# Optimization experiments

Measured on AMD Instinct MI355X. Metric: run time of the kernel, lower is better.

## Reference

```python
import jax, jax.numpy as jnp
import numpy as np

B = 16
C, T, BR, S, SY = 128, 8, 16, 8, 64
INPUT_SIZE = 16384           # layer-1 prev size; also equals C*T*BR for layer 2
SEG_TH = 16.0
BR_TH = 4.0


def setup_inputs() -> dict:
    key = jax.random.key(0)
    kx, k1, k2 = jax.random.split(key, 3)
    # binary {0,1} input, as the module does x.bool()
    x = (jax.random.uniform(kx, (B, INPUT_SIZE)) < 0.5).astype(jnp.float32)
    # sparse connection matrices: synapse index into prev activations, -1 = no synapse
    idx1 = jax.random.randint(k1, (C, T, BR, S, SY), -1, INPUT_SIZE, dtype=jnp.int32)
    idx2 = jax.random.randint(k2, (C, T, BR, S, SY), -1, C * T * BR, dtype=jnp.int32)
    return {"x": x, "idx1": idx1, "idx2": idx2}


def _sparse_layer(prev, idx):
    """prev: (B, N_prev) in {0,1}; idx: (C,T,Br,S,Sy) int, -1 masked.
    Returns branch_on: (B,C,T,Br) in {0,1}."""
    safe = jnp.maximum(idx, 0)
    mask = (idx >= 0).astype(prev.dtype)
    # gather: (B, C, T, Br, S, Sy)
    gathered = prev[:, safe] * mask
    seg_sum = gathered.sum(-1)                      # (B,C,T,Br,S)
    seg_on = (seg_sum >= SEG_TH).astype(prev.dtype)  # threshold 1
    branch_sum = seg_on.sum(-1)                     # (B,C,T,Br)
    return (branch_sum >= BR_TH).astype(prev.dtype)  # threshold 2


def reference(x, idx1, idx2):
    act1 = _sparse_layer(x, idx1)                   # (B,C,T,Br)
    act2 = _sparse_layer(act1.reshape(B, -1), idx2)  # flatten per _forward_sparse
    # trace[-1][:, :, 0].int() -> type index 0 slice: (B, C, Br)
    return act2[:, :, 0].astype(jnp.int32)
```

## Files before the change

kernel.cpp:

```cpp
#include <hip/hip_runtime.h>
#include <stdint.h>

#define NB   16
#define NC   128
#define NT   8
#define NBR  16
#define NS   8
#define NSY  64
#define NIN  16384

__global__ __launch_bounds__(256) void k_pack(const float* __restrict__ x,
                                              uint16_t* __restrict__ xpack) {
    const int i = blockIdx.x * 256 + threadIdx.x;
    uint32_t m = 0;
#pragma unroll
    for (int b = 0; b < NB; ++b)
        m |= (x[b * NIN + i] != 0.0f) ? (1u << b) : 0u;
    xpack[i] = (uint16_t)m;
}

__device__ __forceinline__ void stage(const uint16_t* __restrict__ g,
                                      uint16_t* l, int tid) {
    const uint4* s = (const uint4*)g;
    uint4* d = (uint4*)l;
#pragma unroll
    for (int k = 0; k < 8; ++k) d[k * 256 + tid] = s[k * 256 + tid];
}

__device__ __forceinline__ void pair_masks(const uint16_t* __restrict__ lds16,
                                           uint16_t* __restrict__ s0,
                                           uint16_t* __restrict__ s1,
                                           const int* __restrict__ ip0,
                                           const int* __restrict__ ip1,
                                           int lane, uint32_t sel,
                                           uint32_t& om0, uint32_t& om1) {
    int iv0[NS], iv1[NS];
#pragma unroll
    for (int s = 0; s < NS; ++s) { iv0[s] = ip0[s * NSY]; iv1[s] = ip1[s * NSY]; }
    const uint4* r0 = (const uint4*)(s0 + ((lane >> 4) << 4));
    const uint4* r1 = (const uint4*)(s1 + ((lane >> 4) << 4));
    int bs0 = 0, bs1 = 0;
#pragma unroll
    for (int s = 0; s < NS; ++s) {
        const uint32_t m0 = (uint32_t)lds16[iv0[s] & (NIN - 1)] & ~(uint32_t)(iv0[s] >> 31);
        const uint32_t m1 = (uint32_t)lds16[iv1[s] & (NIN - 1)] & ~(uint32_t)(iv1[s] >> 31);
        __builtin_amdgcn_wave_barrier();
        s0[lane] = (uint16_t)m0;
        s1[lane] = (uint16_t)m1;
        __builtin_amdgcn_wave_barrier();
        const uint4 a0 = r0[0], c0 = r0[1];
        const uint4 a1 = r1[0], c1 = r1[1];
        __builtin_amdgcn_wave_barrier();
        int cnt0 = __popc(a0.x & sel) + __popc(a0.y & sel) + __popc(a0.z & sel) + __popc(a0.w & sel)
                 + __popc(c0.x & sel) + __popc(c0.y & sel) + __popc(c0.z & sel) + __popc(c0.w & sel);
        int cnt1 = __popc(a1.x & sel) + __popc(a1.y & sel) + __popc(a1.z & sel) + __popc(a1.w & sel)
                 + __popc(c1.x & sel) + __popc(c1.y & sel) + __popc(c1.z & sel) + __popc(c1.w & sel);
        cnt0 += __shfl_xor(cnt0, 16);  cnt0 += __shfl_xor(cnt0, 32);
        cnt1 += __shfl_xor(cnt1, 16);  cnt1 += __shfl_xor(cnt1, 32);
        bs0 += (cnt0 >= 16) ? 1 : 0;
        bs1 += (cnt1 >= 16) ? 1 : 0;
    }
    om0 = (uint32_t)(__ballot(bs0 >= 4) & 0xFFFFull);
    om1 = (uint32_t)(__ballot(bs1 >= 4) & 0xFFFFull);
}

__global__ __launch_bounds__(256) void k_layer1(const uint16_t* __restrict__ xpack,
                                                const int* __restrict__ idx1,
                                                uint16_t* __restrict__ act1pack) {
    __shared__ __align__(16) uint16_t lds[NIN];
    __shared__ __align__(16) uint16_t scr[4 * 2 * 64];
    const int tid = threadIdx.x, lane = tid & 63, wave = tid >> 6;
    stage(xpack, lds, tid);
    __syncthreads();
    const uint32_t sel = 0x00010001u << (lane & 15);
    uint16_t* s0 = scr + (wave * 2 + 0) * 64;
    uint16_t* s1 = scr + (wave * 2 + 1) * 64;
#pragma unroll
    for (int it = 0; it < 2; ++it) {
        const int b0 = blockIdx.x * 16 + wave * 4 + it * 2;
        const int b1 = b0 + 1;
        uint32_t om0, om1;
        pair_masks(lds, s0, s1,
                   idx1 + b0 * (NS * NSY) + lane,
                   idx1 + b1 * (NS * NSY) + lane,
                   lane, sel, om0, om1);
        if (lane == 0) { act1pack[b0] = (uint16_t)om0; act1pack[b1] = (uint16_t)om1; }
    }
}

__global__ __launch_bounds__(256) void k_layer2(const uint16_t* __restrict__ act1pack,
                                                const int* __restrict__ idx2,
                                                int* __restrict__ out) {
    __shared__ __align__(16) uint16_t lds[NIN];
    __shared__ __align__(16) uint16_t scr[4 * 2 * 64];
    const int tid = threadIdx.x, lane = tid & 63, wave = tid >> 6;
    stage(act1pack, lds, tid);
    __syncthreads();
    const uint32_t sel = 0x00010001u << (lane & 15);
    uint16_t* s0 = scr + (wave * 2 + 0) * 64;
    uint16_t* s1 = scr + (wave * 2 + 1) * 64;
    const int j0 = blockIdx.x * 8 + wave * 2;
    const int j1 = j0 + 1;
    const int c0 = j0 >> 4, br0 = j0 & 15;
    const int c1 = j1 >> 4, br1 = j1 & 15;
    uint32_t om0, om1;
    pair_masks(lds, s0, s1,
               idx2 + (c0 * (NT * NBR) + br0) * (NS * NSY) + lane,
               idx2 + (c1 * (NT * NBR) + br1) * (NS * NSY) + lane,
               lane, sel, om0, om1);
    if (lane < NB) {
        out[lane * (NC * NBR) + j0] = (int)((om0 >> lane) & 1u);
        out[lane * (NC * NBR) + j1] = (int)((om1 >> lane) & 1u);
    }
}

extern "C" void kernel_launch(void* const* d_in, const int* in_sizes, int n_in,
                              void* d_out, int out_size, void* d_ws, size_t ws_size,
                              hipStream_t stream) {
    const float* x    = (const float*)d_in[0];
    const int*   idx1 = (const int*)d_in[1];
    const int*   idx2 = (const int*)d_in[2];

    uint16_t* xpack    = (uint16_t*)d_ws;
    uint16_t* act1pack = (uint16_t*)((char*)d_ws + 32768);
    int*      out      = (int*)d_out;

    k_pack  <<<NIN / 256, 256, 0, stream>>>(x, xpack);
    k_layer1<<<NIN / 16,  256, 0, stream>>>(xpack, idx1, act1pack);
    k_layer2<<<(NC * NBR) / 8, 256, 0, stream>>>(act1pack, idx2, out);
}
```

Measured before the change: 104.2 us.

## Restructure segment counting: store all segment masks, then split popcount across lanes

```diff
diff --git a/kernel.cpp b/kernel.cpp
--- a/kernel.cpp
+++ b/kernel.cpp
@@ -27,54 +27,63 @@
     for (int k = 0; k < 8; ++k) d[k * 256 + tid] = s[k * 256 + tid];
 }
 
+__device__ __forceinline__ uint32_t compress_even(uint32_t x) {
+    x &= 0x55555555u;
+    x = (x | (x >> 1)) & 0x33333333u;
+    x = (x | (x >> 2)) & 0x0F0F0F0Fu;
+    x = (x | (x >> 4)) & 0x00FF00FFu;
+    x = (x | (x >> 8)) & 0x0000FFFFu;
+    return x;
+}
+
 __device__ __forceinline__ void pair_masks(const uint16_t* __restrict__ lds16,
                                            uint16_t* __restrict__ s0,
                                            uint16_t* __restrict__ s1,
                                            const int* __restrict__ ip0,
                                            const int* __restrict__ ip1,
-                                           int lane, uint32_t sel,
+                                           int lane,
                                            uint32_t& om0, uint32_t& om1) {
     int iv0[NS], iv1[NS];
 #pragma unroll
     for (int s = 0; s < NS; ++s) { iv0[s] = ip0[s * NSY]; iv1[s] = ip1[s * NSY]; }
-    const uint4* r0 = (const uint4*)(s0 + ((lane >> 4) << 4));
-    const uint4* r1 = (const uint4*)(s1 + ((lane >> 4) << 4));
-    int bs0 = 0, bs1 = 0;
 #pragma unroll
     for (int s = 0; s < NS; ++s) {
         const uint32_t m0 = (uint32_t)lds16[iv0[s] & (NIN - 1)] & ~(uint32_t)(iv0[s] >> 31);
         const uint32_t m1 = (uint32_t)lds16[iv1[s] & (NIN - 1)] & ~(uint32_t)(iv1[s] >> 31);
-        __builtin_amdgcn_wave_barrier();
-        s0[lane] = (uint16_t)m0;
-        s1[lane] = (uint16_t)m1;
-        __builtin_amdgcn_wave_barrier();
-        const uint4 a0 = r0[0], c0 = r0[1];
-        const uint4 a1 = r1[0], c1 = r1[1];
-        __builtin_amdgcn_wave_barrier();
-        int cnt0 = __popc(a0.x & sel) + __popc(a0.y & sel) + __popc(a0.z & sel) + __popc(a0.w & sel)
-                 + __popc(c0.x & sel) + __popc(c0.y & sel) + __popc(c0.z & sel) + __popc(c0.w & sel);
-        int cnt1 = __popc(a1.x & sel) + __popc(a1.y & sel) + __popc(a1.z & sel) + __popc(a1.w & sel)
-                 + __popc(c1.x & sel) + __popc(c1.y & sel) + __popc(c1.z & sel) + __popc(c1.w & sel);
-        cnt0 += __shfl_xor(cnt0, 16);  cnt0 += __shfl_xor(cnt0, 32);
-        cnt1 += __shfl_xor(cnt1, 16);  cnt1 += __shfl_xor(cnt1, 32);
-        bs0 += (cnt0 >= 16) ? 1 : 0;
-        bs1 += (cnt1 >= 16) ? 1 : 0;
+        s0[s * 64 + lane] = (uint16_t)m0;
+        s1[s * 64 + lane] = (uint16_t)m1;
     }
-    om0 = (uint32_t)(__ballot(bs0 >= 4) & 0xFFFFull);
-    om1 = (uint32_t)(__ballot(bs1 >= 4) & 0xFFFFull);
+    __builtin_amdgcn_wave_barrier();
+    const int half = lane & 1;
+    const uint32_t sel = 0x00010001u << ((lane >> 1) & 15);
+    const uint4* r = (const uint4*)((lane & 32) ? s1 : s0) + half * 4;
+    int bs = 0;
+#pragma unroll
+    for (int s = 0; s < NS; ++s) {
+        const uint4 a = r[s * 8 + 0], b = r[s * 8 + 1];
+        const uint4 c = r[s * 8 + 2], d = r[s * 8 + 3];
+        int cnt = __popc(a.x & sel) + __popc(a.y & sel) + __popc(a.z & sel) + __popc(a.w & sel)
+                + __popc(b.x & sel) + __popc(b.y & sel) + __popc(b.z & sel) + __popc(b.w & sel)
+                + __popc(c.x & sel) + __popc(c.y & sel) + __popc(c.z & sel) + __popc(c.w & sel)
+                + __popc(d.x & sel) + __popc(d.y & sel) + __popc(d.z & sel) + __popc(d.w & sel);
+        cnt += __shfl_xor(cnt, 1);
+        bs += (cnt >= 16) ? 1 : 0;
+    }
+    const unsigned long long bal = __ballot(bs >= 4);
+    om0 = compress_even((uint32_t)bal);
+    om1 = compress_even((uint32_t)(bal >> 32));
 }
 
-__global__ __launch_bounds__(256) void k_layer1(const uint16_t* __restrict__ xpack,
-                                                const int* __restrict__ idx1,
-                                                uint16_t* __restrict__ act1pack) {
+__global__ __launch_bounds__(256, 4) void k_layer1(const uint16_t* __restrict__ xpack,
+                                                   const int* __restrict__ idx1,
+                                                   uint16_t* __restrict__ act1pack) {
     __shared__ __align__(16) uint16_t lds[NIN];
-    __shared__ __align__(16) uint16_t scr[4 * 2 * 64];
+    __shared__ __align__(16) uint16_t scr[4 * 2 * 512];
     const int tid = threadIdx.x, lane = tid & 63, wave = tid >> 6;
     stage(xpack, lds, tid);
     __syncthreads();
-    const uint32_t sel = 0x00010001u << (lane & 15);
-    uint16_t* s0 = scr + (wave * 2 + 0) * 64;
-    uint16_t* s1 = scr + (wave * 2 + 1) * 64;
+    uint16_t* s0 = scr + (wave * 2 + 0) * 512;
+    uint16_t* s1 = scr + (wave * 2 + 1) * 512;
 #pragma unroll
     for (int it = 0; it < 2; ++it) {
         const int b0 = blockIdx.x * 16 + wave * 4 + it * 2;
@@ -83,22 +92,21 @@
         pair_masks(lds, s0, s1,
                    idx1 + b0 * (NS * NSY) + lane,
                    idx1 + b1 * (NS * NSY) + lane,
-                   lane, sel, om0, om1);
+                   lane, om0, om1);
         if (lane == 0) { act1pack[b0] = (uint16_t)om0; act1pack[b1] = (uint16_t)om1; }
     }
 }
 
-__global__ __launch_bounds__(256) void k_layer2(const uint16_t* __restrict__ act1pack,
-                                                const int* __restrict__ idx2,
-                                                int* __restrict__ out) {
+__global__ __launch_bounds__(256, 4) void k_layer2(const uint16_t* __restrict__ act1pack,
+                                                   const int* __restrict__ idx2,
+                                                   int* __restrict__ out) {
     __shared__ __align__(16) uint16_t lds[NIN];
-    __shared__ __align__(16) uint16_t scr[4 * 2 * 64];
+    __shared__ __align__(16) uint16_t scr[4 * 2 * 512];
     const int tid = threadIdx.x, lane = tid & 63, wave = tid >> 6;
     stage(act1pack, lds, tid);
     __syncthreads();
-    const uint32_t sel = 0x00010001u << (lane & 15);
-    uint16_t* s0 = scr + (wave * 2 + 0) * 64;
-    uint16_t* s1 = scr + (wave * 2 + 1) * 64;
+    uint16_t* s0 = scr + (wave * 2 + 0) * 512;
+    uint16_t* s1 = scr + (wave * 2 + 1) * 512;
     const int j0 = blockIdx.x * 8 + wave * 2;
     const int j1 = j0 + 1;
     const int c0 = j0 >> 4, br0 = j0 & 15;
@@ -107,7 +115,7 @@
     pair_masks(lds, s0, s1,
                idx2 + (c0 * (NT * NBR) + br0) * (NS * NSY) + lane,
                idx2 + (c1 * (NT * NBR) + br1) * (NS * NSY) + lane,
-               lane, sel, om0, om1);
+               lane, om0, om1);
     if (lane < NB) {
         out[lane * (NC * NBR) + j0] = (int)((om0 >> lane) & 1u);
         out[lane * (NC * NBR) + j1] = (int)((om1 >> lane) & 1u);
```

Result: no change. 104.0 us (-0.2%).
